# Kernel optimization log

Hardware: AMD Instinct MI355X
Metric: run time of the kernel (lower is better)

## Reference

```python
import jax, jax.numpy as jnp
import numpy as np

B, S, R, D, A, P = 64, 128, 8, 10000, 10, 256


def setup_inputs() -> dict:
    key = jax.random.key(0)
    ks = jax.random.split(key, 7)
    return {
        "atom_hvs": jax.random.normal(ks[0], (A, D), jnp.float32),
        "pos_hvs": jax.random.normal(ks[1], (S, D), jnp.float32),
        "closure_tag": jax.random.normal(ks[2], (D,), jnp.float32),
        "W": jax.random.normal(ks[3], (P, D), jnp.float32) / np.float32(np.sqrt(D)),
        "b": jax.random.normal(ks[4], (P,), jnp.float32) * 0.01,
        "token_mask": jnp.ones((B, S), jnp.float32),
        "ring_mask": jnp.ones((B, R), jnp.float32),
        "atom_idx": jax.random.randint(ks[5], (B, S), 0, A),
        "ring_pos": jax.random.randint(ks[6], (B, R, 2), 0, S),
    }


def reference(atom_hvs, pos_hvs, closure_tag, W, b, token_mask, ring_mask, atom_idx, ring_pos):
    # HRR bind = circular convolution -> pointwise multiply in rFFT domain.
    # Bundle = sum; by linearity we sum in the frequency domain and do a
    # single irfft per molecule (same math as per-token conv + add).
    d = atom_hvs.shape[-1]
    Fa = jnp.fft.rfft(atom_hvs, axis=-1)          # [A, F]
    Fp = jnp.fft.rfft(pos_hvs, axis=-1)           # [S, F]
    Fc = jnp.fft.rfft(closure_tag)                # [F]

    s = atom_idx.shape[1]
    tok = Fa[atom_idx] * Fp[None, :s, :]          # [B, S, F] gather+bind
    freq = jnp.sum(token_mask[..., None] * tok, axis=1)   # [B, F] bundle

    ring = Fp[ring_pos[..., 0]] * Fp[ring_pos[..., 1]] * Fc  # [B, R, F]
    freq = freq + jnp.sum(ring_mask[..., None] * ring, axis=1)

    mol_hv = jnp.fft.irfft(freq, n=d, axis=-1)    # [B, D]
    return mol_hv @ W.T + b                       # [B, proj_dim]
```

## Files before the change

kernel.cpp:

```cpp
#include <hip/hip_runtime.h>

#define PI2 6.28318530717958647692f

#define NSIG 139
#define FS   5120

__global__ __launch_bounds__(256) void k_fwd(
                     const float* __restrict__ atom, const float* __restrict__ pos,
                     const float* __restrict__ clo, float2* __restrict__ spec) {
  __shared__ float lds[10000];
  unsigned sig = blockIdx.x, q = blockIdx.y;
  unsigned k1base = q * 10u;
  unsigned nk1 = (k1base + 10u <= 51u) ? 10u : (51u - k1base);
  const float* xb = (sig < 128u) ? (pos + sig * 10000u)
                   : ((sig < 138u) ? (atom + (sig - 128u) * 10000u) : clo);
  int tid = threadIdx.x;

  {
    float* csA = lds;
    float* csB = lds + 2500;
    float* csG = lds + 5000;
    float* csH = lds + 7500;
    for (int t2 = tid; t2 < 625; t2 += 256) {
      const float* p = xb + (t2 / 25) * 100 + (t2 % 25) * 4;
      float4 x0 = *(const float4*)(p);
      float4 x1 = *(const float4*)(p + 2500);
      float4 x2 = *(const float4*)(p + 5000);
      float4 x3 = *(const float4*)(p + 7500);
      float4 A, B, G, H;
      A.x = (x0.x + x2.x) + (x1.x + x3.x);
      A.y = (x0.y + x2.y) + (x1.y + x3.y);
      A.z = (x0.z + x2.z) + (x1.z + x3.z);
      A.w = (x0.w + x2.w) + (x1.w + x3.w);
      B.x = (x0.x + x2.x) - (x1.x + x3.x);
      B.y = (x0.y + x2.y) - (x1.y + x3.y);
      B.z = (x0.z + x2.z) - (x1.z + x3.z);
      B.w = (x0.w + x2.w) - (x1.w + x3.w);
      G.x = x0.x - x2.x;  G.y = x0.y - x2.y;
      G.z = x0.z - x2.z;  G.w = x0.w - x2.w;
      H.x = x1.x - x3.x;  H.y = x1.y - x3.y;
      H.z = x1.z - x3.z;  H.w = x1.w - x3.w;
      *(float4*)(csA + t2 * 4) = A;
      *(float4*)(csB + t2 * 4) = B;
      *(float4*)(csG + t2 * 4) = G;
      *(float4*)(csH + t2 * 4) = H;
    }
  }
  __syncthreads();

  unsigned ntile1 = nk1 * 25u;
  unsigned k1l = tid / 25u, n2q = (unsigned)tid % 25u, n2 = n2q * 4u;
  bool have = (unsigned)tid < ntile1;
  unsigned k1 = k1base + k1l;
  float resA[8], resB[8];
  if (have) {
    float cth, sth;
    __sincosf(PI2 * (float)k1 * 0.01f, &sth, &cth);
    unsigned m = k1 & 3u;
    const float4* creP = (const float4*)((m == 0u) ? lds
                          : (m == 2u) ? (lds + 2500) : (lds + 5000)) + n2q;
    const float4* cimP = (const float4*)(lds + 7500) + n2q;
    float im_mul = (m == 1u) ? 1.0f : (m == 3u) ? -1.0f : 0.0f;
    float c = 1.0f, s = 0.0f;
    float ar[4] = {}, as[4] = {};
#pragma unroll 5
    for (int n1l = 0; n1l < 25; ++n1l) {
      float4 Cre = creP[n1l * 25];
      float4 Cim = cimP[n1l * 25];
      float se = im_mul * s, ce = im_mul * c;
      ar[0] += Cre.x * c - Cim.x * se;  as[0] += Cim.x * ce + Cre.x * s;
      ar[1] += Cre.y * c - Cim.y * se;  as[1] += Cim.y * ce + Cre.y * s;
      ar[2] += Cre.z * c - Cim.z * se;  as[2] += Cim.z * ce + Cre.z * s;
      ar[3] += Cre.w * c - Cim.w * se;  as[3] += Cim.w * ce + Cre.w * s;
      float cn = c * cth - s * sth;
      float sn = s * cth + c * sth;
      c = cn; s = sn;
    }
    unsigned rb = (100u - k1) % 100u;
#pragma unroll
    for (int j = 0; j < 4; ++j) {
      float swA, cwA, swB, cwB;
      __sincosf(PI2 * (float)((n2 + j) * k1) * 1e-4f, &swA, &cwA);
      __sincosf(PI2 * (float)((n2 + j) * rb) * 1e-4f, &swB, &cwB);
      resA[2 * j + 0] = ar[j] * cwA - as[j] * swA;
      resA[2 * j + 1] = -(as[j] * cwA + ar[j] * swA);
      resB[2 * j + 0] = ar[j] * cwB + as[j] * swB;
      resB[2 * j + 1] = as[j] * cwB - ar[j] * swB;
    }
  }
  __syncthreads();
  float* xs = lds;
  if (have) {
    float* pA = xs + k1l * 200u + n2 * 2u;
    float* pB = xs + (nk1 + k1l) * 200u + n2 * 2u;
    *(float4*)(pA + 0) = make_float4(resA[0], resA[1], resA[2], resA[3]);
    *(float4*)(pA + 4) = make_float4(resA[4], resA[5], resA[6], resA[7]);
    *(float4*)(pB + 0) = make_float4(resB[0], resB[1], resB[2], resB[3]);
    *(float4*)(pB + 4) = make_float4(resB[4], resB[5], resB[6], resB[7]);
  }
  __syncthreads();

  unsigned nrow = 2u * nk1;
  float* cse = lds + 4000;
  float* cso = lds + 6000;
  for (int t3 = tid; t3 < (int)(nrow * 25u); t3 += 256) {
    const float* br = xs + (t3 / 25) * 200;
    int n2l = t3 % 25;
    float2 b0 = *(const float2*)(br + 2 * n2l);
    float2 b1 = *(const float2*)(br + 2 * (25 + n2l));
    float2 b2 = *(const float2*)(br + 2 * (50 + n2l));
    float2 b3 = *(const float2*)(br + 2 * (75 + n2l));
    float4 e, o;
    e.x = (b0.x + b2.x) + (b1.x + b3.x);
    e.y = (b0.y + b2.y) + (b1.y + b3.y);
    e.z = (b0.x + b2.x) - (b1.x + b3.x);
    e.w = (b0.y + b2.y) - (b1.y + b3.y);
    o.x = b0.x - b2.x;
    o.y = b1.y - b3.y;
    o.z = b0.y - b2.y;
    o.w = b1.x - b3.x;
    *(float4*)(cse + t3 * 4) = e;
    *(float4*)(cso + t3 * 4) = o;
  }
  __syncthreads();

  unsigned ntile3 = nrow * 26u;
  for (unsigned t = tid; t < ntile3; t += 256u) {
    unsigned lr = t / 26u, k2 = (t % 26u) * 2u;
    unsigned gk1 = (lr < nk1) ? (k1base + lr) : ((100u - (k1base + (lr - nk1))) % 100u);
    float cthA, sthA, cthB, sthB;
    __sincosf(PI2 * (float)k2 * 0.01f, &sthA, &cthA);
    __sincosf(PI2 * (float)(k2 + 1) * 0.01f, &sthB, &cthB);
    bool hi = (k2 & 2u) != 0u;
    float sq = hi ? -1.0f : 1.0f;
    const float4* pe = (const float4*)(cse + lr * 100);
    const float4* po = (const float4*)(cso + lr * 100);
    float cA = 1.0f, sA = 0.0f, cB = 1.0f, sB = 0.0f;
    float reA = 0.f, imA = 0.f, reB = 0.f, imB = 0.f;
#pragma unroll 5
    for (int n2l = 0; n2l < 25; ++n2l) {
      float4 e = pe[n2l];
      float4 o = po[n2l];
      float car = hi ? e.z : e.x;
      float cai = hi ? e.w : e.y;
      float cbr = o.x + sq * o.y;
      float cbi = o.z - sq * o.w;
      reA += car * cA + cai * sA;  imA += cai * cA - car * sA;
      reB += cbr * cB + cbi * sB;  imB += cbi * cB - cbr * sB;
      float cA1 = cA * cthA - sA * sthA, sA1 = sA * cthA + cA * sthA;
      float cB1 = cB * cthB - sB * sthB, sB1 = sB * cthB + cB * sthB;
      cA = cA1; sA = sA1; cB = cB1; sB = sB1;
    }
    unsigned kA = gk1 + 100u * k2;
    unsigned kB = gk1 + 100u * (k2 + 1);
    if (kA <= 5000u) spec[sig * FS + kA] = make_float2(reA, imA);
    if (kB <= 5000u) spec[sig * FS + kB] = make_float2(reB, imB);
  }
}

__global__ __launch_bounds__(256) void k_mix(const float2* __restrict__ spec,
                      const float* __restrict__ tmask, const float* __restrict__ rmask,
                      const int* __restrict__ aidx, const int* __restrict__ rpos,
                      float2* __restrict__ G) {
  __shared__ float2 FaS[10][128];
  __shared__ float2 FcS[128];
  __shared__ float tmS[4][128];
  __shared__ int   aiS[4][128];
  __shared__ float rmS[4][8];
  __shared__ int   rpS[4][8][2];
  __shared__ float2 red[2][4][128];
  int tid = threadIdx.x;
  int kl = tid & 127, half = tid >> 7;
  int k = blockIdx.x * 128 + kl;
  int kc = k > 5000 ? 5000 : k;
  int b0 = blockIdx.y * 4;
  for (int i = tid; i < 10 * 128; i += 256) {
    int a = i >> 7, kk = i & 127;
    int kg = blockIdx.x * 128 + kk; if (kg > 5000) kg = 5000;
    FaS[a][kk] = spec[(128 + a) * FS + kg];
  }
  if (tid < 128) FcS[tid] = spec[138 * FS + kc];
  for (int i = tid; i < 4 * 128; i += 256) {
    int bb = i >> 7, ss = i & 127;
    tmS[bb][ss] = tmask[(b0 + bb) * 128 + ss];
    aiS[bb][ss] = aidx[(b0 + bb) * 128 + ss];
  }
  if (tid < 32) {
    int bb = tid >> 3, rr = tid & 7;
    rmS[bb][rr] = rmask[(b0 + bb) * 8 + rr];
    rpS[bb][rr][0] = rpos[((b0 + bb) * 8 + rr) * 2 + 0];
    rpS[bb][rr][1] = rpos[((b0 + bb) * 8 + rr) * 2 + 1];
  }
  __syncthreads();
  float fr[4] = {}, fi[4] = {};
  int sbase = half * 64;
#pragma unroll 8
  for (int si = 0; si < 64; ++si) {
    int s = sbase + si;
    float2 fp = spec[s * FS + kc];
#pragma unroll
    for (int b = 0; b < 4; ++b) {
      int a = aiS[b][s];
      float tm = tmS[b][s];
      float2 fa = FaS[a][kl];
      fr[b] += tm * (fa.x * fp.x - fa.y * fp.y);
      fi[b] += tm * (fa.x * fp.y + fa.y * fp.x);
    }
  }
  float2 fc = FcS[kl];
#pragma unroll
  for (int rr = 0; rr < 4; ++rr) {
    int r = half * 4 + rr;
#pragma unroll
    for (int b = 0; b < 4; ++b) {
      int p0 = rpS[b][r][0], p1 = rpS[b][r][1];
      float rm = rmS[b][r];
      float2 f0 = spec[p0 * FS + kc];
      float2 f1 = spec[p1 * FS + kc];
      float tr = f0.x * f1.x - f0.y * f1.y;
      float ti = f0.x * f1.y + f0.y * f1.x;
      fr[b] += rm * (tr * fc.x - ti * fc.y);
      fi[b] += rm * (tr * fc.y + ti * fc.x);
    }
  }
#pragma unroll
  for (int b = 0; b < 4; ++b) red[half][b][kl] = make_float2(fr[b], fi[b]);
  __syncthreads();
  if (k <= 5000) {
#pragma unroll
    for (int j = 0; j < 2; ++j) {
      int b = half + 2 * j;
      float R = red[0][b][kl].x + red[1][b][kl].x;
      float I = red[0][b][kl].y + red[1][b][kl].y;
      if (k == 0 || k == 5000) I = 0.0f;
      G[(size_t)(b0 + b) * 10000 + k] = make_float2(R, I);
      if (k >= 1 && k <= 4999)
        G[(size_t)(b0 + b) * 10000 + (10000 - k)] = make_float2(R, -I);
    }
  }
}

__global__ __launch_bounds__(256) void k_i1(const float2* __restrict__ G,
                                            float2* __restrict__ Bi) {
  __shared__ float lds[10400];
  unsigned sig = blockIdx.x;
  const float* gp = (const float*)(G + sig * 10000u);
  int tid = threadIdx.x;
  float* c0v = lds;
  float* c2v = lds + 2600;
  float* cpr = lds + 5200;
  float* cqt = lds + 7800;
  for (int t2 = tid; t2 < 650; t2 += 256) {
    const float* p = gp + (t2 / 26) * 200 + (t2 % 26) * 4;
    float4 g0 = *(const float4*)(p);
    float4 g1 = *(const float4*)(p + 5000);
    float4 g2 = *(const float4*)(p + 10000);
    float4 g3 = *(const float4*)(p + 15000);
    float4 a, b, pr, qt;
    a.x = (g0.x + g2.x) + (g1.x + g3.x);
    a.y = (g0.y + g2.y) + (g1.y + g3.y);
    a.z = (g0.z + g2.z) + (g1.z + g3.z);
    a.w = (g0.w + g2.w) + (g1.w + g3.w);
    b.x = (g0.x + g2.x) - (g1.x + g3.x);
    b.y = (g0.y + g2.y) - (g1.y + g3.y);
    b.z = (g0.z + g2.z) - (g1.z + g3.z);
    b.w = (g0.w + g2.w) - (g1.w + g3.w);
    pr.x = g0.x - g2.x;  pr.y = g0.y - g2.y;
    pr.z = g0.z - g2.z;  pr.w = g0.w - g2.w;
    qt.x = g1.y - g3.y;  qt.y = g1.x - g3.x;
    qt.z = g1.w - g3.w;  qt.w = g1.z - g3.z;
    *(float4*)(c0v + t2 * 4) = a;
    *(float4*)(c2v + t2 * 4) = b;
    *(float4*)(cpr + t2 * 4) = pr;
    *(float4*)(cqt + t2 * 4) = qt;
  }
  __syncthreads();
  unsigned t = blockIdx.y * 256u + tid;
  if (t >= 2600u) return;
  unsigned m1 = t / 26u, n2p = t % 26u, n2 = n2p * 2u;
  float cth, sth;
  __sincosf(PI2 * (float)m1 * 0.01f, &sth, &cth);
  unsigned m = m1 & 3u;
  const float4* pe = (const float4*)((m == 0u) ? c0v : (m == 2u) ? c2v : cpr) + n2p;
  const float4* pq = (const float4*)cqt + n2p;
  float qmul = (m == 1u) ? -1.0f : (m == 3u) ? 1.0f : 0.0f;
  float c = 1.0f, s = 0.0f;
  float reA = 0.f, imA = 0.f, reB = 0.f, imB = 0.f;
#pragma unroll 5
  for (int n1l = 0; n1l < 25; ++n1l) {
    float4 ev = pe[n1l * 26];
    float4 qv = pq[n1l * 26];
    float gx = ev.x + qmul * qv.x;
    float gy = ev.y - qmul * qv.y;
    float gz = ev.z + qmul * qv.z;
    float gw = ev.w - qmul * qv.w;
    reA += gx * c - gy * s;  imA += gy * c + gx * s;
    reB += gz * c - gw * s;  imB += gw * c + gz * s;
    float cn = c * cth - s * sth;
    float sn = s * cth + c * sth;
    c = cn; s = sn;
  }
  float w0 = (n2 == 0u || n2 == 50u) ? 0.5f : 1.0f;
  float w1 = (n2 == 50u) ? 0.0f : 1.0f;
  float sw0, cw0, sw1, cw1;
  __sincosf(PI2 * (float)(n2 * m1) * 1e-4f, &sw0, &cw0);
  __sincosf(PI2 * (float)((n2 + 1u) * m1) * 1e-4f, &sw1, &cw1);
  float4 outv;
  outv.x = (reA * cw0 - imA * sw0) * w0;
  outv.y = (imA * cw0 + reA * sw0) * w0;
  outv.z = (reB * cw1 - imB * sw1) * w1;
  outv.w = (imB * cw1 + reB * sw1) * w1;
  *(float4*)((float*)Bi + (sig * 5200u + m1 * 52u + n2) * 2) = outv;
}

__global__ __launch_bounds__(256) void k_i2(const float2* __restrict__ Bi,
                                            float* __restrict__ mol) {
  unsigned sig = blockIdx.x, q = blockIdx.y;
  int tid = threadIdx.x;
  unsigned t = blockIdx.z * 256u + tid;
  if (t >= 1250u) return;
  unsigned m1l = t / 50u;
  unsigned m2 = (t % 50u) * 2u;
  const float* b0 = (const float*)Bi + sig * 10400u + q * 2600u + m1l * 104u;
  float cthA, sthA, cthB, sthB;
  __sincosf(PI2 * (float)m2 * 0.01f, &sthA, &cthA);
  __sincosf(PI2 * (float)(m2 + 1u) * 0.01f, &sthB, &cthB);
  float cA = 1.0f, sA = 0.0f, cB = 1.0f, sB = 0.0f;
  float r0 = 0.f, r1 = 0.f;
#pragma unroll 4
  for (int jj = 0; jj < 26; ++jj) {
    int n2i = 2 * jj;
    const float4 v0 = *(const float4*)(b0 + 2 * n2i);
    r0 += v0.x * cA - v0.y * sA;
    r1 += v0.x * cB - v0.y * sB;
    float cA1 = cA * cthA - sA * sthA, sA1 = sA * cthA + cA * sthA;
    float cB1 = cB * cthB - sB * sthB, sB1 = sB * cthB + cB * sthB;
    r0 += v0.z * cA1 - v0.w * sA1;
    r1 += v0.z * cB1 - v0.w * sB1;
    cA = cA1 * cthA - sA1 * sthA; sA = sA1 * cthA + cA1 * sthA;
    cB = cB1 * cthB - sB1 * sthB; sB = sB1 * cthB + cB1 * sthB;
  }
  unsigned m1 = q * 25u + m1l;
  mol[sig * 10000u + m1 + 100u * m2] = r0 * 2e-4f;
  mol[sig * 10000u + m1 + 100u * (m2 + 1u)] = r1 * 2e-4f;
}

__global__ __launch_bounds__(512) void k_proj(const float* __restrict__ mol,
                                              const float* __restrict__ W,
                                              float* __restrict__ part) {
  __shared__ float molS[40 * 66];
  __shared__ float WS[40][258];
  int tid = threadIdx.x;
  int d0 = blockIdx.x * 40;
  for (int i = tid; i < 40 * 64; i += 512) {
    int b = i / 40, dl = i % 40;
    molS[dl * 66 + b] = mol[(size_t)b * 10000 + d0 + dl];
  }
  for (int i = tid; i < 40 * 256; i += 512) {
    int p = i / 40, dl = i % 40;
    WS[dl][p] = W[(size_t)p * 10000 + d0 + dl];
  }
  __syncthreads();
  int p0 = (tid & 127) * 2;
  int bh = (tid >> 7) * 16;
  float acc[2][16] = {};
#pragma unroll 4
  for (int dl = 0; dl < 40; ++dl) {
    const float2 wv = *(const float2*)(&WS[dl][p0]);
    const float2* m2p = (const float2*)(molS + dl * 66 + bh);
#pragma unroll
    for (int qq = 0; qq < 8; ++qq) {
      float2 mv = m2p[qq];
      acc[0][2 * qq + 0] += wv.x * mv.x;  acc[1][2 * qq + 0] += wv.y * mv.x;
      acc[0][2 * qq + 1] += wv.x * mv.y;  acc[1][2 * qq + 1] += wv.y * mv.y;
    }
  }
#pragma unroll
  for (int b = 0; b < 16; ++b)
    *(float2*)(part + (size_t)blockIdx.x * 16384 + (bh + b) * 256 + p0) =
        make_float2(acc[0][b], acc[1][b]);
}

__global__ __launch_bounds__(256) void k_red(const float* __restrict__ part,
                                             const float* __restrict__ bias,
                                             float* __restrict__ out) {
  __shared__ float red[4][64];
  int tid = threadIdx.x;
  int pl = tid & 63, cg = tid >> 6;
  int b = blockIdx.x;
  int p = blockIdx.y * 64 + pl;
  float acc = 0.0f;
#pragma unroll 8
  for (int ch = cg; ch < 250; ch += 4)
    acc += part[(size_t)ch * 16384 + b * 256 + p];
  red[cg][pl] = acc;
  __syncthreads();
  if (tid < 64)
    out[b * 256 + p] = red[0][pl] + red[1][pl] + red[2][pl] + red[3][pl] + bias[p];
}

extern "C" void kernel_launch(void* const* d_in, const int* in_sizes, int n_in,
                              void* d_out, int out_size, void* d_ws, size_t ws_size,
                              hipStream_t stream) {
  const float* atom  = (const float*)d_in[0];
  const float* pos   = (const float*)d_in[1];
  const float* clo   = (const float*)d_in[2];
  const float* W     = (const float*)d_in[3];
  const float* bias  = (const float*)d_in[4];
  const float* tmask = (const float*)d_in[5];
  const float* rmask = (const float*)d_in[6];
  const int*   aidx  = (const int*)d_in[7];
  const int*   rpos  = (const int*)d_in[8];
  float* out = (float*)d_out;

  char* ws = (char*)d_ws;
  size_t off = 0;
  auto alloc = [&](size_t n) { off = (off + 255) & ~(size_t)255; size_t o = off; off += n; return o; };
  char* regA   = ws + alloc(16777216);
  float2* Bi   = (float2*)regA;
  float*  part = (float*)regA;
  float2* spec = (float2*)(ws + alloc((size_t)NSIG * FS * 8));
  float2* G    = (float2*)(ws + alloc((size_t)64 * 10000 * 8));
  float*  mol  = (float*)(ws + alloc((size_t)64 * 10000 * 4));

  k_fwd<<<dim3(NSIG, 6), dim3(256), 0, stream>>>(atom, pos, clo, spec);
  k_mix<<<dim3(40, 16), dim3(256), 0, stream>>>(spec, tmask, rmask, aidx, rpos, G);
  k_i1<<<dim3(64, 11), dim3(256), 0, stream>>>(G, Bi);
  k_i2<<<dim3(64, 4, 5), dim3(256), 0, stream>>>(Bi, mol);
  k_proj<<<dim3(250), dim3(512), 0, stream>>>(mol, W, part);
  k_red<<<dim3(64, 4), dim3(256), 0, stream>>>(part, bias, out);
}
```

Before: 166.8 us.

## Exploit DFT half-symmetry in inverse stages and retile mixing kernel

The inverse-FFT stages now compute two output frequencies per thread. In k_i1 the m1 and m1+50 outputs come from a shared twiddle recurrence with an alternating sign. In k_i2 the even and odd partial sums are combined to produce the outputs at m2 and m2+50. Together this halves the thread counts and the redundant loads and twiddle work. Separately, k_mix is retiled to handle 64 frequencies and 8 batches per block, with a 4-way split over sequence positions, to reuse each spec load across more batches. The trade-off is higher register pressure and fewer blocks in the inverse kernels.

```diff
diff --git a/kernel.cpp b/kernel.cpp
--- a/kernel.cpp
+++ b/kernel.cpp
@@ -162,44 +162,44 @@
                       const float* __restrict__ tmask, const float* __restrict__ rmask,
                       const int* __restrict__ aidx, const int* __restrict__ rpos,
                       float2* __restrict__ G) {
-  __shared__ float2 FaS[10][128];
-  __shared__ float2 FcS[128];
-  __shared__ float tmS[4][128];
-  __shared__ int   aiS[4][128];
-  __shared__ float rmS[4][8];
-  __shared__ int   rpS[4][8][2];
-  __shared__ float2 red[2][4][128];
-  int tid = threadIdx.x;
-  int kl = tid & 127, half = tid >> 7;
-  int k = blockIdx.x * 128 + kl;
+  __shared__ float2 FaS[10][64];
+  __shared__ float2 FcS[64];
+  __shared__ float tmS[8][128];
+  __shared__ int   aiS[8][128];
+  __shared__ float rmS[8][8];
+  __shared__ int   rpS[8][8][2];
+  __shared__ float2 red[4][8][64];
+  int tid = threadIdx.x;
+  int kl = tid & 63, grp = tid >> 6;
+  int k = blockIdx.x * 64 + kl;
   int kc = k > 5000 ? 5000 : k;
-  int b0 = blockIdx.y * 4;
-  for (int i = tid; i < 10 * 128; i += 256) {
-    int a = i >> 7, kk = i & 127;
-    int kg = blockIdx.x * 128 + kk; if (kg > 5000) kg = 5000;
+  int b0 = blockIdx.y * 8;
+  for (int i = tid; i < 640; i += 256) {
+    int a = i >> 6, kk = i & 63;
+    int kg = blockIdx.x * 64 + kk; if (kg > 5000) kg = 5000;
     FaS[a][kk] = spec[(128 + a) * FS + kg];
   }
-  if (tid < 128) FcS[tid] = spec[138 * FS + kc];
-  for (int i = tid; i < 4 * 128; i += 256) {
+  if (tid < 64) FcS[tid] = spec[138 * FS + kc];
+  for (int i = tid; i < 8 * 128; i += 256) {
     int bb = i >> 7, ss = i & 127;
     tmS[bb][ss] = tmask[(b0 + bb) * 128 + ss];
     aiS[bb][ss] = aidx[(b0 + bb) * 128 + ss];
   }
-  if (tid < 32) {
+  if (tid < 64) {
     int bb = tid >> 3, rr = tid & 7;
     rmS[bb][rr] = rmask[(b0 + bb) * 8 + rr];
     rpS[bb][rr][0] = rpos[((b0 + bb) * 8 + rr) * 2 + 0];
     rpS[bb][rr][1] = rpos[((b0 + bb) * 8 + rr) * 2 + 1];
   }
   __syncthreads();
-  float fr[4] = {}, fi[4] = {};
-  int sbase = half * 64;
-#pragma unroll 8
-  for (int si = 0; si < 64; ++si) {
+  float fr[8] = {}, fi[8] = {};
+  int sbase = grp * 32;
+#pragma unroll 4
+  for (int si = 0; si < 32; ++si) {
     int s = sbase + si;
     float2 fp = spec[s * FS + kc];
 #pragma unroll
-    for (int b = 0; b < 4; ++b) {
+    for (int b = 0; b < 8; ++b) {
       int a = aiS[b][s];
       float tm = tmS[b][s];
       float2 fa = FaS[a][kl];
@@ -209,10 +209,10 @@
   }
   float2 fc = FcS[kl];
 #pragma unroll
-  for (int rr = 0; rr < 4; ++rr) {
-    int r = half * 4 + rr;
-#pragma unroll
-    for (int b = 0; b < 4; ++b) {
+  for (int rr = 0; rr < 2; ++rr) {
+    int r = grp * 2 + rr;
+#pragma unroll
+    for (int b = 0; b < 8; ++b) {
       int p0 = rpS[b][r][0], p1 = rpS[b][r][1];
       float rm = rmS[b][r];
       float2 f0 = spec[p0 * FS + kc];
@@ -224,18 +224,20 @@
     }
   }
 #pragma unroll
-  for (int b = 0; b < 4; ++b) red[half][b][kl] = make_float2(fr[b], fi[b]);
-  __syncthreads();
-  if (k <= 5000) {
-#pragma unroll
-    for (int j = 0; j < 2; ++j) {
-      int b = half + 2 * j;
-      float R = red[0][b][kl].x + red[1][b][kl].x;
-      float I = red[0][b][kl].y + red[1][b][kl].y;
-      if (k == 0 || k == 5000) I = 0.0f;
-      G[(size_t)(b0 + b) * 10000 + k] = make_float2(R, I);
-      if (k >= 1 && k <= 4999)
-        G[(size_t)(b0 + b) * 10000 + (10000 - k)] = make_float2(R, -I);
+  for (int b = 0; b < 8; ++b) red[grp][b][kl] = make_float2(fr[b], fi[b]);
+  __syncthreads();
+#pragma unroll
+  for (int j = 0; j < 2; ++j) {
+    int slot = j * 256 + tid;
+    int b = slot >> 6, kk = slot & 63;
+    int kg = blockIdx.x * 64 + kk;
+    if (kg <= 5000) {
+      float R = red[0][b][kk].x + red[1][b][kk].x + red[2][b][kk].x + red[3][b][kk].x;
+      float I = red[0][b][kk].y + red[1][b][kk].y + red[2][b][kk].y + red[3][b][kk].y;
+      if (kg == 0 || kg == 5000) I = 0.0f;
+      G[(size_t)(b0 + b) * 10000 + kg] = make_float2(R, I);
+      if (kg >= 1 && kg <= 4999)
+        G[(size_t)(b0 + b) * 10000 + (10000 - kg)] = make_float2(R, -I);
     }
   }
 }
@@ -276,41 +278,62 @@
   }
   __syncthreads();
   unsigned t = blockIdx.y * 256u + tid;
-  if (t >= 2600u) return;
+  if (t >= 1300u) return;
   unsigned m1 = t / 26u, n2p = t % 26u, n2 = n2p * 2u;
   float cth, sth;
   __sincosf(PI2 * (float)m1 * 0.01f, &sth, &cth);
   unsigned m = m1 & 3u;
-  const float4* pe = (const float4*)((m == 0u) ? c0v : (m == 2u) ? c2v : cpr) + n2p;
-  const float4* pq = (const float4*)cqt + n2p;
+  const float4* pe  = (const float4*)((m == 0u) ? c0v : (m == 2u) ? c2v : cpr) + n2p;
+  const float4* pe2 = (const float4*)((m == 0u) ? c2v : (m == 2u) ? c0v : cpr) + n2p;
+  const float4* pq  = (const float4*)cqt + n2p;
   float qmul = (m == 1u) ? -1.0f : (m == 3u) ? 1.0f : 0.0f;
-  float c = 1.0f, s = 0.0f;
+  float qmul2 = -qmul;
+  float c = 1.0f, s = 0.0f, sg = 1.0f;
   float reA = 0.f, imA = 0.f, reB = 0.f, imB = 0.f;
+  float reA2 = 0.f, imA2 = 0.f, reB2 = 0.f, imB2 = 0.f;
 #pragma unroll 5
   for (int n1l = 0; n1l < 25; ++n1l) {
     float4 ev = pe[n1l * 26];
+    float4 e2 = pe2[n1l * 26];
     float4 qv = pq[n1l * 26];
-    float gx = ev.x + qmul * qv.x;
-    float gy = ev.y - qmul * qv.y;
-    float gz = ev.z + qmul * qv.z;
-    float gw = ev.w - qmul * qv.w;
+    float gx = ev.x + qmul * qv.x,  gy = ev.y - qmul * qv.y;
+    float gz = ev.z + qmul * qv.z,  gw = ev.w - qmul * qv.w;
+    float hx = e2.x + qmul2 * qv.x, hy = e2.y - qmul2 * qv.y;
+    float hz = e2.z + qmul2 * qv.z, hw = e2.w - qmul2 * qv.w;
     reA += gx * c - gy * s;  imA += gy * c + gx * s;
     reB += gz * c - gw * s;  imB += gw * c + gz * s;
+    float cs = sg * c, ss = sg * s;
+    reA2 += hx * cs - hy * ss;  imA2 += hy * cs + hx * ss;
+    reB2 += hz * cs - hw * ss;  imB2 += hw * cs + hz * ss;
     float cn = c * cth - s * sth;
     float sn = s * cth + c * sth;
-    c = cn; s = sn;
+    c = cn; s = sn; sg = -sg;
   }
   float w0 = (n2 == 0u || n2 == 50u) ? 0.5f : 1.0f;
   float w1 = (n2 == 50u) ? 0.0f : 1.0f;
-  float sw0, cw0, sw1, cw1;
-  __sincosf(PI2 * (float)(n2 * m1) * 1e-4f, &sw0, &cw0);
-  __sincosf(PI2 * (float)((n2 + 1u) * m1) * 1e-4f, &sw1, &cw1);
-  float4 outv;
-  outv.x = (reA * cw0 - imA * sw0) * w0;
-  outv.y = (imA * cw0 + reA * sw0) * w0;
-  outv.z = (reB * cw1 - imB * sw1) * w1;
-  outv.w = (imB * cw1 + reB * sw1) * w1;
-  *(float4*)((float*)Bi + (sig * 5200u + m1 * 52u + n2) * 2) = outv;
+  {
+    float sw0, cw0, sw1, cw1;
+    __sincosf(PI2 * (float)(n2 * m1) * 1e-4f, &sw0, &cw0);
+    __sincosf(PI2 * (float)((n2 + 1u) * m1) * 1e-4f, &sw1, &cw1);
+    float4 outv;
+    outv.x = (reA * cw0 - imA * sw0) * w0;
+    outv.y = (imA * cw0 + reA * sw0) * w0;
+    outv.z = (reB * cw1 - imB * sw1) * w1;
+    outv.w = (imB * cw1 + reB * sw1) * w1;
+    *(float4*)((float*)Bi + (sig * 5200u + m1 * 52u + n2) * 2) = outv;
+  }
+  {
+    unsigned m1b = m1 + 50u;
+    float sw0, cw0, sw1, cw1;
+    __sincosf(PI2 * (float)(n2 * m1b) * 1e-4f, &sw0, &cw0);
+    __sincosf(PI2 * (float)((n2 + 1u) * m1b) * 1e-4f, &sw1, &cw1);
+    float4 outv;
+    outv.x = (reA2 * cw0 - imA2 * sw0) * w0;
+    outv.y = (imA2 * cw0 + reA2 * sw0) * w0;
+    outv.z = (reB2 * cw1 - imB2 * sw1) * w1;
+    outv.w = (imB2 * cw1 + reB2 * sw1) * w1;
+    *(float4*)((float*)Bi + (sig * 5200u + m1b * 52u + n2) * 2) = outv;
+  }
 }
 
 __global__ __launch_bounds__(256) void k_i2(const float2* __restrict__ Bi,
@@ -318,31 +341,33 @@
   unsigned sig = blockIdx.x, q = blockIdx.y;
   int tid = threadIdx.x;
   unsigned t = blockIdx.z * 256u + tid;
-  if (t >= 1250u) return;
-  unsigned m1l = t / 50u;
-  unsigned m2 = (t % 50u) * 2u;
-  const float* b0 = (const float*)Bi + sig * 10400u + q * 2600u + m1l * 104u;
+  if (t >= 625u) return;
+  unsigned m1l = t / 25u;
+  unsigned m2 = (t % 25u) * 2u;
+  const float* bp = (const float*)Bi + sig * 10400u + q * 2600u + m1l * 104u;
   float cthA, sthA, cthB, sthB;
   __sincosf(PI2 * (float)m2 * 0.01f, &sthA, &cthA);
   __sincosf(PI2 * (float)(m2 + 1u) * 0.01f, &sthB, &cthB);
   float cA = 1.0f, sA = 0.0f, cB = 1.0f, sB = 0.0f;
-  float r0 = 0.f, r1 = 0.f;
+  float r0e = 0.f, r0o = 0.f, r1e = 0.f, r1o = 0.f;
 #pragma unroll 4
   for (int jj = 0; jj < 26; ++jj) {
-    int n2i = 2 * jj;
-    const float4 v0 = *(const float4*)(b0 + 2 * n2i);
-    r0 += v0.x * cA - v0.y * sA;
-    r1 += v0.x * cB - v0.y * sB;
+    const float4 v0 = *(const float4*)(bp + 4 * jj);
+    r0e += v0.x * cA - v0.y * sA;
+    r1e += v0.x * cB - v0.y * sB;
     float cA1 = cA * cthA - sA * sthA, sA1 = sA * cthA + cA * sthA;
     float cB1 = cB * cthB - sB * sthB, sB1 = sB * cthB + cB * sthB;
-    r0 += v0.z * cA1 - v0.w * sA1;
-    r1 += v0.z * cB1 - v0.w * sB1;
+    r0o += v0.z * cA1 - v0.w * sA1;
+    r1o += v0.z * cB1 - v0.w * sB1;
     cA = cA1 * cthA - sA1 * sthA; sA = sA1 * cthA + cA1 * sthA;
     cB = cB1 * cthB - sB1 * sthB; sB = sB1 * cthB + cB1 * sthB;
   }
   unsigned m1 = q * 25u + m1l;
-  mol[sig * 10000u + m1 + 100u * m2] = r0 * 2e-4f;
-  mol[sig * 10000u + m1 + 100u * (m2 + 1u)] = r1 * 2e-4f;
+  float* mp = mol + sig * 10000u + m1;
+  mp[100u * m2]          = (r0e + r0o) * 2e-4f;
+  mp[100u * (m2 + 1u)]   = (r1e + r1o) * 2e-4f;
+  mp[100u * (m2 + 50u)]  = (r0e - r0o) * 2e-4f;
+  mp[100u * (m2 + 51u)]  = (r1e - r1o) * 2e-4f;
 }
 
 __global__ __launch_bounds__(512) void k_proj(const float* __restrict__ mol,
@@ -424,9 +449,9 @@
   float*  mol  = (float*)(ws + alloc((size_t)64 * 10000 * 4));
 
   k_fwd<<<dim3(NSIG, 6), dim3(256), 0, stream>>>(atom, pos, clo, spec);
-  k_mix<<<dim3(40, 16), dim3(256), 0, stream>>>(spec, tmask, rmask, aidx, rpos, G);
-  k_i1<<<dim3(64, 11), dim3(256), 0, stream>>>(G, Bi);
-  k_i2<<<dim3(64, 4, 5), dim3(256), 0, stream>>>(Bi, mol);
+  k_mix<<<dim3(80, 8), dim3(256), 0, stream>>>(spec, tmask, rmask, aidx, rpos, G);
+  k_i1<<<dim3(64, 6), dim3(256), 0, stream>>>(G, Bi);
+  k_i2<<<dim3(64, 4, 3), dim3(256), 0, stream>>>(Bi, mol);
   k_proj<<<dim3(250), dim3(512), 0, stream>>>(mol, W, part);
   k_red<<<dim3(64, 4), dim3(256), 0, stream>>>(part, bias, out);
 }
```

Measured after the change: 161.4 us. 3.3% less time.
